# Optimization experiments

Measured on AMD Instinct MI355X. Metric: run time of the kernel, lower is better.

The kernel has to match this reference:

```python
import jax, jax.numpy as jnp
import numpy as np

N_NODES = 50000
N_EDGES = 800000
D_FEAT = 128
DIM_H = 128
N_LAYERS = 3
N_CLASSES = 10
N_GRAPHS = 512


def setup_inputs() -> dict:
    key = jax.random.key(0)
    ks = jax.random.split(key, 8)
    x = jax.random.normal(ks[0], (N_NODES, D_FEAT), dtype=jnp.float32)
    W = jax.random.normal(ks[1], (N_LAYERS, DIM_H, DIM_H), dtype=jnp.float32) * 0.1
    b = jnp.zeros((N_LAYERS, DIM_H), dtype=jnp.float32)
    lin_w = jax.random.normal(ks[2], (DIM_H, N_CLASSES), dtype=jnp.float32) * 0.1
    lin_b = jnp.zeros((N_CLASSES,), dtype=jnp.float32)
    edge_index = jax.random.randint(ks[3], (2, N_EDGES), 0, N_NODES, dtype=jnp.int64)
    batch = jnp.sort(jax.random.randint(ks[4], (N_NODES,), 0, N_GRAPHS, dtype=jnp.int64))
    return {"x": x, "W": W, "b": b, "lin_w": lin_w, "lin_b": lin_b,
            "edge_index": edge_index, "batch": batch, "num_layers": N_LAYERS}


def _gcn_norm(edge_index, n_nodes):
    # add self loops (PyG GCNConv default), then symmetric normalization
    loop = jnp.arange(n_nodes, dtype=edge_index.dtype)
    src = jnp.concatenate([edge_index[0], loop])  # [E+N]
    dst = jnp.concatenate([edge_index[1], loop])
    deg = jax.ops.segment_sum(jnp.ones_like(dst, dtype=jnp.float32), dst,
                              num_segments=n_nodes)
    dinv = jnp.where(deg > 0, jax.lax.rsqrt(deg), 0.0)
    norm = dinv[src] * dinv[dst]  # [E+N]
    return src, dst, norm


def _gcn_conv(h, Wi, bi, src, dst, norm, n_nodes):
    h = h @ Wi                       # [N, dim_h] dense GEMM
    msg = h[src] * norm[:, None]     # gather + scale, [E+N, dim_h]
    out = jax.ops.segment_sum(msg, dst, num_segments=n_nodes)  # scatter-add
    return out + bi


def reference(x, W, b, lin_w, lin_b, edge_index, batch, num_layers):
    n_nodes = x.shape[0]
    src, dst, norm = _gcn_norm(edge_index, n_nodes)
    h = x
    for i in range(num_layers):
        h = jax.nn.relu(_gcn_conv(h, W[i], b[i], src, dst, norm, n_nodes))
    # global mean pool over graph ids
    sums = jax.ops.segment_sum(h, batch, num_segments=N_GRAPHS)          # [G, dim_h]
    cnts = jax.ops.segment_sum(jnp.ones((n_nodes,), h.dtype), batch,
                               num_segments=N_GRAPHS)
    hG = sums / jnp.maximum(cnts, 1.0)[:, None]
    # dropout is identity at eval; num_layers > 1 branch applies the linear head
    logits = hG @ lin_w + lin_b
    return hG, jax.nn.log_softmax(logits, axis=1)
```

## Files before the change

### kernel.cpp

```cpp
#include <hip/hip_runtime.h>
#include <hip/hip_bf16.h>
#include <hip/hip_fp8.h>

#define NN 50000
#define NE 800000
#define FD 128
#define NG 512
#define NC 10
#define NL 3
#define CAP 64
#define E1_B 3125
#define GEMM_B 782
#define CVT_B 128
#define FRONT_B 4550
#define PATCH_B 12500

typedef unsigned short u16;
typedef unsigned char u8;
typedef unsigned int u32;
typedef short bf16x8 __attribute__((ext_vector_type(8)));
typedef float f32x4 __attribute__((ext_vector_type(4)));
typedef float f32x2 __attribute__((ext_vector_type(2)));

__device__ __forceinline__ float b2f(u16 v) {
    union { u32 u; float f; } c; c.u = ((u32)v) << 16; return c.f;
}
__device__ __forceinline__ u16 f2b(float f) {
    __hip_bfloat16 h = __float2bfloat16(f);
    return *(u16*)&h;
}
__device__ __forceinline__ float p2f(u8 b) {
    __hip_fp8_e4m3 h; h.__x = b; return (float)h;
}
__device__ __forceinline__ u8 f2p(float f) {
    __hip_fp8_e4m3 h(f); return h.__x;
}

#if defined(__has_builtin)
#if __has_builtin(__builtin_amdgcn_cvt_pk_f32_fp8)
#define HAVE_PKCVT 1
#endif
#endif
template<bool HI>
__device__ __forceinline__ f32x2 pkcvt(u32 u) {
#ifdef HAVE_PKCVT
    return __builtin_amdgcn_cvt_pk_f32_fp8((int)u, HI);
#else
    f32x2 r;
    r[0] = p2f((u8)(HI ? (u >> 16) : u));
    r[1] = p2f((u8)(HI ? (u >> 24) : (u >> 8)));
    return r;
#endif
}

__global__ __launch_bounds__(256) void k_front(const int* __restrict__ src,
                                               const int* __restrict__ dst,
                                               int* __restrict__ cnt,
                                               int* __restrict__ bkt,
                                               const float* __restrict__ W,
                                               u16* __restrict__ wt,
                                               const float* __restrict__ x,
                                               u8* __restrict__ Bout) {
    const int bid = blockIdx.x;
    const int r5 = bid % 5;
    const int q5 = bid / 5;
    if (r5 != 0) {
        const int sid = q5 * 4 + (r5 - 1);
        if (sid >= E1_B) return;
        const int e = sid * 256 + threadIdx.x;
        const int d = dst[e];
        const int slot = atomicAdd(&cnt[d], 1);
        if (slot < CAP) bkt[d * CAP + slot] = src[e];
    } else if (q5 < GEMM_B) {
        const int wid = q5 * 4 + (threadIdx.x >> 6);
        if (wid >= 3125) return;
        const int row0 = wid * 16;
        const int lane = threadIdx.x & 63;
        const int m = lane & 15;
        const int q = lane >> 4;
        f32x4 acc[8];
#pragma unroll
        for (int ct = 0; ct < 8; ++ct) acc[ct] = (f32x4){0.f, 0.f, 0.f, 0.f};
        const float* arow = x + (size_t)(row0 + m) * FD + q * 8;
        const float* wbase = W + (size_t)q * 8 * FD + m;
#pragma unroll
        for (int kb = 0; kb < 4; ++kb) {
            const float4 p0 = *(const float4*)(arow + kb * 32);
            const float4 p1 = *(const float4*)(arow + kb * 32 + 4);
            bf16x8 af;
            af[0] = (short)f2b(p0.x); af[1] = (short)f2b(p0.y);
            af[2] = (short)f2b(p0.z); af[3] = (short)f2b(p0.w);
            af[4] = (short)f2b(p1.x); af[5] = (short)f2b(p1.y);
            af[6] = (short)f2b(p1.z); af[7] = (short)f2b(p1.w);
#pragma unroll
            for (int ct = 0; ct < 8; ++ct) {
                const float* wp = wbase + (size_t)kb * 32 * FD + ct * 16;
                bf16x8 bf;
#pragma unroll
                for (int j = 0; j < 8; ++j)
                    bf[j] = (short)f2b(wp[(size_t)j * FD]);
                acc[ct] = __builtin_amdgcn_mfma_f32_16x16x32_bf16(af, bf,
                                                                  acc[ct], 0, 0, 0);
            }
        }
#pragma unroll
        for (int ct = 0; ct < 8; ++ct)
#pragma unroll
            for (int r = 0; r < 4; ++r)
                Bout[(size_t)(row0 + q * 4 + r) * FD + ct * 16 + m] =
                    f2p(acc[ct][r]);
    } else {
        const int c = (q5 - GEMM_B) * 256 + threadIdx.x + FD * FD;
        const int l = c >> 14, rr = c & 16383, k = rr >> 7, n = rr & 127;
        wt[(l << 14) + n * FD + k] = f2b(W[c]);
    }
}

__global__ __launch_bounds__(256) void k_patch(const int* __restrict__ cnt,
                                               int* __restrict__ bkt) {
    const int i = blockIdx.x * 256 + threadIdx.x;
    const int d = i >> 6;
    const int s = i & 63;
    if (s < cnt[d]) {
        const int v = bkt[i];
        const u32 w = (u32)f2b(rsqrtf((float)(cnt[v] + 1)));
        bkt[i] = (int)(((u32)v & 0xFFFFu) | (w << 16));
    }
}

template<bool W8>
__device__ __forceinline__ float4 gather_node(const int rs, const int re,
                                              const int* __restrict__ bkt,
                                              const u8* __restrict__ B,
                                              const float di, const int n,
                                              const float4 bb, const int f) {
    const u32 us = *(const u32*)(B + (size_t)n * FD + f);
    f32x2 aL0 = {0.f, 0.f}, aL1 = {0.f, 0.f}, aL2 = {0.f, 0.f}, aL3 = {0.f, 0.f};
    f32x2 aH0 = {0.f, 0.f}, aH1 = {0.f, 0.f}, aH2 = {0.f, 0.f}, aH3 = {0.f, 0.f};
    int e = rs;
    if (W8) {
        for (; e + 8 <= re; e += 8) {
            const int4 p0 = *(const int4*)(bkt + e);
            const int4 p1 = *(const int4*)(bkt + e + 4);
            const u32 r0 = *(const u32*)(B + (size_t)(p0.x & 0xFFFF) * FD + f);
            const u32 r1 = *(const u32*)(B + (size_t)(p0.y & 0xFFFF) * FD + f);
            const u32 r2 = *(const u32*)(B + (size_t)(p0.z & 0xFFFF) * FD + f);
            const u32 r3 = *(const u32*)(B + (size_t)(p0.w & 0xFFFF) * FD + f);
            const u32 r4 = *(const u32*)(B + (size_t)(p1.x & 0xFFFF) * FD + f);
            const u32 r5 = *(const u32*)(B + (size_t)(p1.y & 0xFFFF) * FD + f);
            const u32 r6 = *(const u32*)(B + (size_t)(p1.z & 0xFFFF) * FD + f);
            const u32 r7 = *(const u32*)(B + (size_t)(p1.w & 0xFFFF) * FD + f);
            const float w0 = b2f((u16)((u32)p0.x >> 16));
            const float w1 = b2f((u16)((u32)p0.y >> 16));
            const float w2 = b2f((u16)((u32)p0.z >> 16));
            const float w3 = b2f((u16)((u32)p0.w >> 16));
            const float w4 = b2f((u16)((u32)p1.x >> 16));
            const float w5 = b2f((u16)((u32)p1.y >> 16));
            const float w6 = b2f((u16)((u32)p1.z >> 16));
            const float w7 = b2f((u16)((u32)p1.w >> 16));
            aL0 += pkcvt<false>(r0) * w0; aH0 += pkcvt<true>(r0) * w0;
            aL1 += pkcvt<false>(r1) * w1; aH1 += pkcvt<true>(r1) * w1;
            aL2 += pkcvt<false>(r2) * w2; aH2 += pkcvt<true>(r2) * w2;
            aL3 += pkcvt<false>(r3) * w3; aH3 += pkcvt<true>(r3) * w3;
            aL0 += pkcvt<false>(r4) * w4; aH0 += pkcvt<true>(r4) * w4;
            aL1 += pkcvt<false>(r5) * w5; aH1 += pkcvt<true>(r5) * w5;
            aL2 += pkcvt<false>(r6) * w6; aH2 += pkcvt<true>(r6) * w6;
            aL3 += pkcvt<false>(r7) * w7; aH3 += pkcvt<true>(r7) * w7;
        }
    }
    for (; e + 4 <= re; e += 4) {
        const int4 p0 = *(const int4*)(bkt + e);
        const u32 r0 = *(const u32*)(B + (size_t)(p0.x & 0xFFFF) * FD + f);
        const u32 r1 = *(const u32*)(B + (size_t)(p0.y & 0xFFFF) * FD + f);
        const u32 r2 = *(const u32*)(B + (size_t)(p0.z & 0xFFFF) * FD + f);
        const u32 r3 = *(const u32*)(B + (size_t)(p0.w & 0xFFFF) * FD + f);
        const float w0 = b2f((u16)((u32)p0.x >> 16));
        const float w1 = b2f((u16)((u32)p0.y >> 16));
        const float w2 = b2f((u16)((u32)p0.z >> 16));
        const float w3 = b2f((u16)((u32)p0.w >> 16));
        aL0 += pkcvt<false>(r0) * w0; aH0 += pkcvt<true>(r0) * w0;
        aL1 += pkcvt<false>(r1) * w1; aH1 += pkcvt<true>(r1) * w1;
        aL2 += pkcvt<false>(r2) * w2; aH2 += pkcvt<true>(r2) * w2;
        aL3 += pkcvt<false>(r3) * w3; aH3 += pkcvt<true>(r3) * w3;
    }
    for (; e < re; ++e) {
        const int pk = bkt[e];
        const u32 r0 = *(const u32*)(B + (size_t)(pk & 0xFFFF) * FD + f);
        const float w0 = b2f((u16)((u32)pk >> 16));
        aL0 += pkcvt<false>(r0) * w0; aH0 += pkcvt<true>(r0) * w0;
    }
    aL0 += pkcvt<false>(us) * di;
    aH0 += pkcvt<true>(us) * di;
    const f32x2 L = (aL0 + aL1) + (aL2 + aL3);
    const f32x2 H = (aH0 + aH1) + (aH2 + aH3);
    float4 r;
    r.x = fmaxf(fmaf(L[0], di, bb.x), 0.f);
    r.y = fmaxf(fmaf(L[1], di, bb.y), 0.f);
    r.z = fmaxf(fmaf(H[0], di, bb.z), 0.f);
    r.w = fmaxf(fmaf(H[1], di, bb.w), 0.f);
    return r;
}

__global__ __launch_bounds__(512) void k_gg(const int* __restrict__ cnt,
                                            const int* __restrict__ bkt,
                                            const u8* __restrict__ Bin,
                                            const float* __restrict__ bias,
                                            const u16* __restrict__ WTn,
                                            u8* __restrict__ Bout) {
    __shared__ u16 sA[16][FD + 8];
    const int tid = threadIdx.x;
    const int wave = tid >> 6;
    const int lane = tid & 63;
    const int nb = blockIdx.x * 16;
    {
        const int half = lane >> 5;
        const int n = nb + wave * 2 + half;
        const int f = (lane & 31) * 4;
        const int cn = cnt[n];
        const int rs = n * CAP;
        const float di = rsqrtf((float)(cn + 1));
        const float4 bb = *(const float4*)(bias + f);
        const float4 r = gather_node<true>(rs, rs + cn, bkt, Bin, di, n, bb, f);
        ushort4 o;
        o.x = f2b(r.x); o.y = f2b(r.y); o.z = f2b(r.z); o.w = f2b(r.w);
        *(ushort4*)&sA[wave * 2 + half][f] = o;
    }
    __syncthreads();
    const int ct = wave;
    const int m = lane & 15;
    const int q = lane >> 4;
    f32x4 acc = (f32x4){0.f, 0.f, 0.f, 0.f};
    const u16* wrow = WTn + (size_t)m * FD + q * 8 + (size_t)ct * 16 * FD;
#pragma unroll
    for (int kb = 0; kb < 4; ++kb) {
        bf16x8 af = *(const bf16x8*)&sA[m][q * 8 + kb * 32];
        bf16x8 bf = *(const bf16x8*)(wrow + kb * 32);
        acc = __builtin_amdgcn_mfma_f32_16x16x32_bf16(af, bf, acc, 0, 0, 0);
    }
#pragma unroll
    for (int r = 0; r < 4; ++r)
        Bout[(size_t)(nb + q * 4 + r) * FD + ct * 16 + m] = f2p(acc[r]);
}

__global__ __launch_bounds__(1024) void k_gpool(const int* __restrict__ cnt,
                                                const int* __restrict__ bkt,
                                                const u8* __restrict__ B,
                                                const float* __restrict__ bias,
                                                const int* __restrict__ batch,
                                                const float* __restrict__ lin_w,
                                                const float* __restrict__ lin_b,
                                                float* __restrict__ out) {
    __shared__ float sfeat[32][FD + 4];
    __shared__ float hm[FD];
    __shared__ int bnd[2];
    __shared__ float part2[2 * NC];
    const int g = blockIdx.x;
    const int tid = threadIdx.x;
    const int lane = tid & 63;
    const int slot = (tid >> 6) * 2 + (lane >> 5);
    const int f = (lane & 31) * 4;
    if (tid < 2) {
        const int key = g + tid;
        int lo = 0, hi = NN;
        while (lo < hi) {
            const int mid = (lo + hi) >> 1;
            if (batch[mid] < key) lo = mid + 1; else hi = mid;
        }
        bnd[tid] = lo;
    }
    __syncthreads();
    const int r0 = bnd[0], r1 = bnd[1];
    const float4 bb = *(const float4*)(bias + f);
    float s0 = 0.f, s1 = 0.f, s2 = 0.f, s3 = 0.f;
    for (int r = r0 + slot; r < r1; r += 32) {
        const int cn = cnt[r];
        const int rs = r * CAP;
        const float di = rsqrtf((float)(cn + 1));
        const float4 v = gather_node<false>(rs, rs + cn, bkt, B, di, r, bb, f);
        s0 += v.x; s1 += v.y; s2 += v.z; s3 += v.w;
    }
    sfeat[slot][f] = s0;
    sfeat[slot][f + 1] = s1;
    sfeat[slot][f + 2] = s2;
    sfeat[slot][f + 3] = s3;
    __syncthreads();
    if (tid < 128) {
        float tot = 0.f;
#pragma unroll
        for (int s = 0; s < 32; ++s) tot += sfeat[s][tid];
        const float mean = tot / fmaxf((float)(r1 - r0), 1.0f);
        hm[tid] = mean;
        out[(size_t)g * FD + tid] = mean;
    }
    __syncthreads();
    if (tid < 128) {
        const float hv = hm[tid];
        const int wv = tid >> 6;
#pragma unroll
        for (int c = 0; c < NC; ++c) {
            float p = hv * lin_w[tid * NC + c];
#pragma unroll
            for (int o = 32; o > 0; o >>= 1) p += __shfl_down(p, o, 64);
            if ((tid & 63) == 0) part2[c * 2 + wv] = p;
        }
    }
    __syncthreads();
    if (tid == 0) {
        float lg[NC];
        float m = -1e30f;
#pragma unroll
        for (int c = 0; c < NC; ++c) {
            lg[c] = part2[2 * c] + part2[2 * c + 1] + lin_b[c];
            m = fmaxf(m, lg[c]);
        }
        float s = 0.f;
#pragma unroll
        for (int c = 0; c < NC; ++c) s += expf(lg[c] - m);
        const float lse = m + logf(s);
        float* o = out + (size_t)NG * FD + (size_t)g * NC;
#pragma unroll
        for (int c = 0; c < NC; ++c) o[c] = lg[c] - lse;
    }
}

extern "C" void kernel_launch(void* const* d_in, const int* in_sizes, int n_in,
                              void* d_out, int out_size, void* d_ws, size_t ws_size,
                              hipStream_t stream) {
    const float* x     = (const float*)d_in[0];
    const float* W     = (const float*)d_in[1];
    const float* bias  = (const float*)d_in[2];
    const float* lin_w = (const float*)d_in[3];
    const float* lin_b = (const float*)d_in[4];
    const int*   src   = (const int*)d_in[5];
    const int*   dst   = src + NE;
    const int*   batch = (const int*)d_in[6];

    u8*    B0     = (u8*)d_ws;
    u8*    B1     = B0 + (size_t)NN * FD;
    u16*   WT     = (u16*)(B1 + (size_t)NN * FD);
    int*   bkt    = (int*)(WT + (size_t)NL * FD * FD);
    int*   cnt    = bkt + (size_t)NN * CAP;
    float* out    = (float*)d_out;

    (void)hipMemsetAsync(cnt, 0, NN * sizeof(int), stream);
    k_front<<<FRONT_B, 256, 0, stream>>>(src, dst, cnt, bkt, W, WT, x, B0);
    k_patch<<<PATCH_B, 256, 0, stream>>>(cnt, bkt);

    k_gg<<<NN / 16, 512, 0, stream>>>(cnt, bkt, B0, bias,
                                      WT + (size_t)1 * FD * FD, B1);
    k_gg<<<NN / 16, 512, 0, stream>>>(cnt, bkt, B1, bias + FD,
                                      WT + (size_t)2 * FD * FD, B0);
    k_gpool<<<NG, 1024, 0, stream>>>(cnt, bkt, B0, bias + 2 * FD,
                                     batch, lin_w, lin_b, out);
}
```

Baseline: 228.1 us.

## Partition edge bucketing by destination range per XCD to localize atomics

The edge-bucketing part of the front kernel now assigns blocks to eight bins, apparently matching the round-robin mapping of blocks to XCDs. Each bin scans every 1024-edge chunk but only inserts edges whose destination falls in its 6250-node range, so the atomic counters and bucket writes for a node range stay in one XCD's L2. The GEMM and weight-convert blocks are interleaved every ninth block. In exchange, every edge's destination index is read eight times, and insertion order within buckets changes.

Result: no change. 228.7 us (+0.3%).

```diff
diff --git a/kernel.cpp b/kernel.cpp
--- a/kernel.cpp
+++ b/kernel.cpp
@@ -9,10 +9,13 @@
 #define NC 10
 #define NL 3
 #define CAP 64
-#define E1_B 3125
 #define GEMM_B 782
 #define CVT_B 128
-#define FRONT_B 4550
+#define COMP_B 910
+#define CHUNKS 782
+#define NXCD 8
+#define NODES_PER_XCD 6250
+#define FRONT_B 8190
 #define PATCH_B 12500
 
 typedef unsigned short u16;
@@ -62,57 +65,71 @@
                                                const float* __restrict__ x,
                                                u8* __restrict__ Bout) {
     const int bid = blockIdx.x;
-    const int r5 = bid % 5;
-    const int q5 = bid / 5;
-    if (r5 != 0) {
-        const int sid = q5 * 4 + (r5 - 1);
-        if (sid >= E1_B) return;
-        const int e = sid * 256 + threadIdx.x;
-        const int d = dst[e];
-        const int slot = atomicAdd(&cnt[d], 1);
-        if (slot < CAP) bkt[d * CAP + slot] = src[e];
-    } else if (q5 < GEMM_B) {
-        const int wid = q5 * 4 + (threadIdx.x >> 6);
-        if (wid >= 3125) return;
-        const int row0 = wid * 16;
-        const int lane = threadIdx.x & 63;
-        const int m = lane & 15;
-        const int q = lane >> 4;
-        f32x4 acc[8];
-#pragma unroll
-        for (int ct = 0; ct < 8; ++ct) acc[ct] = (f32x4){0.f, 0.f, 0.f, 0.f};
-        const float* arow = x + (size_t)(row0 + m) * FD + q * 8;
-        const float* wbase = W + (size_t)q * 8 * FD + m;
-#pragma unroll
-        for (int kb = 0; kb < 4; ++kb) {
-            const float4 p0 = *(const float4*)(arow + kb * 32);
-            const float4 p1 = *(const float4*)(arow + kb * 32 + 4);
-            bf16x8 af;
-            af[0] = (short)f2b(p0.x); af[1] = (short)f2b(p0.y);
-            af[2] = (short)f2b(p0.z); af[3] = (short)f2b(p0.w);
-            af[4] = (short)f2b(p1.x); af[5] = (short)f2b(p1.y);
-            af[6] = (short)f2b(p1.z); af[7] = (short)f2b(p1.w);
-#pragma unroll
-            for (int ct = 0; ct < 8; ++ct) {
-                const float* wp = wbase + (size_t)kb * 32 * FD + ct * 16;
-                bf16x8 bf;
-#pragma unroll
-                for (int j = 0; j < 8; ++j)
-                    bf[j] = (short)f2b(wp[(size_t)j * FD]);
-                acc[ct] = __builtin_amdgcn_mfma_f32_16x16x32_bf16(af, bf,
-                                                                  acc[ct], 0, 0, 0);
+    if (bid % 9 == 0) {
+        const int q = bid / 9;
+        if (q < GEMM_B) {
+            const int wid = q * 4 + (threadIdx.x >> 6);
+            if (wid >= 3125) return;
+            const int row0 = wid * 16;
+            const int lane = threadIdx.x & 63;
+            const int m = lane & 15;
+            const int qq = lane >> 4;
+            f32x4 acc[8];
+#pragma unroll
+            for (int ct = 0; ct < 8; ++ct) acc[ct] = (f32x4){0.f, 0.f, 0.f, 0.f};
+            const float* arow = x + (size_t)(row0 + m) * FD + qq * 8;
+            const float* wbase = W + (size_t)qq * 8 * FD + m;
+#pragma unroll
+            for (int kb = 0; kb < 4; ++kb) {
+                const float4 p0 = *(const float4*)(arow + kb * 32);
+                const float4 p1 = *(const float4*)(arow + kb * 32 + 4);
+                bf16x8 af;
+                af[0] = (short)f2b(p0.x); af[1] = (short)f2b(p0.y);
+                af[2] = (short)f2b(p0.z); af[3] = (short)f2b(p0.w);
+                af[4] = (short)f2b(p1.x); af[5] = (short)f2b(p1.y);
+                af[6] = (short)f2b(p1.z); af[7] = (short)f2b(p1.w);
+#pragma unroll
+                for (int ct = 0; ct < 8; ++ct) {
+                    const float* wp = wbase + (size_t)kb * 32 * FD + ct * 16;
+                    bf16x8 bf;
+#pragma unroll
+                    for (int j = 0; j < 8; ++j)
+                        bf[j] = (short)f2b(wp[(size_t)j * FD]);
+                    acc[ct] = __builtin_amdgcn_mfma_f32_16x16x32_bf16(af, bf,
+                                                                      acc[ct], 0, 0, 0);
+                }
             }
-        }
-#pragma unroll
-        for (int ct = 0; ct < 8; ++ct)
-#pragma unroll
-            for (int r = 0; r < 4; ++r)
-                Bout[(size_t)(row0 + q * 4 + r) * FD + ct * 16 + m] =
-                    f2p(acc[ct][r]);
-    } else {
-        const int c = (q5 - GEMM_B) * 256 + threadIdx.x + FD * FD;
-        const int l = c >> 14, rr = c & 16383, k = rr >> 7, n = rr & 127;
-        wt[(l << 14) + n * FD + k] = f2b(W[c]);
+#pragma unroll
+            for (int ct = 0; ct < 8; ++ct)
+#pragma unroll
+                for (int r = 0; r < 4; ++r)
+                    Bout[(size_t)(row0 + qq * 4 + r) * FD + ct * 16 + m] =
+                        f2p(acc[ct][r]);
+        } else {
+            const int c = (q - GEMM_B) * 256 + threadIdx.x + FD * FD;
+            const int l = c >> 14, rr = c & 16383, k = rr >> 7, n = rr & 127;
+            wt[(l << 14) + n * FD + k] = f2b(W[c]);
+        }
+        return;
+    }
+    const int bin = bid & 7;
+    const int t = bid >> 3;
+    const int m0 = 9 * bin;
+    const int c9 = (bid > m0) ? ((bid - m0 - 1) / 72 + 1) : 0;
+    const int chunk = t - c9;
+    if (chunk >= CHUNKS) return;
+    const int e0 = chunk * 1024 + (threadIdx.x << 2);
+    if (e0 >= NE) return;
+    const int4 d4 = *(const int4*)(dst + e0);
+    const int dd[4] = {d4.x, d4.y, d4.z, d4.w};
+#pragma unroll
+    for (int j = 0; j < 4; ++j) {
+        const int d = dd[j];
+        if ((u32)d / (u32)NODES_PER_XCD == (u32)bin) {
+            const int s = src[e0 + j];
+            const int slot = atomicAdd(&cnt[d], 1);
+            if (slot < CAP) bkt[d * CAP + slot] = s;
+        }
     }
 }
 
```
